# Performance work log

Measured on AMD Instinct MI355X. Metric: run time of the kernel, lower is better.

Reference implementation:

```python
import jax, jax.numpy as jnp
import numpy as np

NTYPES = 2
MAXNEI = 128      # maxNeighborNum
M2 = 16
NPER = 256        # atoms per type
B = 4
EMB = [25, 50, 100]
FIT_IN = M2 * EMB[-1]  # 1600
FH = 240


def setup_inputs() -> dict:
    key = jax.random.key(0)
    ks = jax.random.split(key, 16)
    s = 0.1
    inp = {
        "Ri": jax.random.normal(ks[0], (B, NTYPES * NPER, NTYPES * MAXNEI, 4), jnp.float32),
        "emb_W0": jax.random.normal(ks[1], (4, 1, EMB[0]), jnp.float32) * s,
        "emb_b0": jax.random.normal(ks[2], (4, EMB[0]), jnp.float32) * s,
        "emb_W1": jax.random.normal(ks[3], (4, EMB[0], EMB[1]), jnp.float32) * s,
        "emb_b1": jax.random.normal(ks[4], (4, EMB[1]), jnp.float32) * s,
        "emb_W2": jax.random.normal(ks[5], (4, EMB[1], EMB[2]), jnp.float32) * s,
        "emb_b2": jax.random.normal(ks[6], (4, EMB[2]), jnp.float32) * s,
        "fit_W0": jax.random.normal(ks[7], (2, FIT_IN, FH), jnp.float32) * 0.02,
        "fit_b0": jax.random.normal(ks[8], (2, FH), jnp.float32) * s,
        "fit_W1": jax.random.normal(ks[9], (2, FH, FH), jnp.float32) * 0.05,
        "fit_b1": jax.random.normal(ks[10], (2, FH), jnp.float32) * s,
        "fit_W2": jax.random.normal(ks[11], (2, FH, FH), jnp.float32) * 0.05,
        "fit_b2": jax.random.normal(ks[12], (2, FH), jnp.float32) * s,
        "fit_W3": jax.random.normal(ks[13], (2, FH, 1), jnp.float32) * 0.05,
        "fit_b3": jax.random.normal(ks[14], (2, 1), jnp.float32),
    }
    return inp


def _emb(s, W0, b0, W1, b1, W2, b2):
    # DeepMD-style embedding MLP with doubling resnet skips (1->25->50->100)
    h0 = jnp.tanh(s @ W0 + b0)
    h1 = jnp.tanh(h0 @ W1 + b1) + jnp.concatenate([h0, h0], axis=-1)
    h2 = jnp.tanh(h1 @ W2 + b2) + jnp.concatenate([h1, h1], axis=-1)
    return h2


def _fit(d, W0, b0, W1, b1, W2, b2, W3, b3):
    h = jnp.tanh(d @ W0 + b0)
    h = jnp.tanh(h @ W1 + b1) + h   # resnet skip (equal dims)
    h = jnp.tanh(h @ W2 + b2) + h
    return h @ W3 + b3              # [B, N, 1]


def reference(Ri, emb_W0, emb_b0, emb_W1, emb_b1, emb_W2, emb_b2,
              fit_W0, fit_b0, fit_W1, fit_b1, fit_W2, fit_b2, fit_W3, fit_b3):
    type_nums = NTYPES
    Ei_blocks = []
    for i in range(NTYPES):                      # center-atom type
        Ri_i = Ri[:, i * NPER:(i + 1) * NPER]    # [B, NPER, NTYPES*M, 4]
        xyz = None
        for j in range(NTYPES):                  # neighbor type
            blk = Ri_i[:, :, j * MAXNEI:(j + 1) * MAXNEI, :]  # [B,N,M,4]
            S = blk[..., 0:1]                                  # [B,N,M,1]
            e = i * NTYPES + j
            G = _emb(S, emb_W0[e], emb_b0[e], emb_W1[e], emb_b1[e],
                     emb_W2[e], emb_b2[e])                     # [B,N,M,100]
            tmp = jnp.einsum('bnmc,bnmg->bncg', blk, G)        # [B,N,4,100]
            xyz = tmp if xyz is None else xyz + tmp
        xyz = xyz / (MAXNEI * type_nums)
        xyz_b = xyz[..., :M2]                                  # [B,N,4,16]
        DR = jnp.einsum('bncg,bnch->bngh', xyz, xyz_b)         # [B,N,100,16]
        DR = DR.reshape(B, NPER, FIT_IN)
        Ei_i = _fit(DR, fit_W0[i], fit_b0[i], fit_W1[i], fit_b1[i],
                    fit_W2[i], fit_b2[i], fit_W3[i], fit_b3[i])  # [B,N,1]
        Ei_blocks.append(Ei_i)
    Ei = jnp.concatenate(Ei_blocks, axis=1)     # [B, natoms_sum, 1]
    return Ei[..., 0]                            # per-atom energies [B, natoms_sum]
```

## Files before the change

### kernel.cpp

```cpp
#include <hip/hip_runtime.h>
#include <hip/hip_bf16.h>

#define FH 240
#define FIT_IN 1600
#define NK 2048
#define TLO -16.0f
#define TINVH 64.0f

typedef _Float16 h8 __attribute__((ext_vector_type(8)));
typedef float f4v __attribute__((ext_vector_type(4)));

__device__ __forceinline__ float fast_tanh(float x) {
    float e2 = __builtin_amdgcn_exp2f(x * 2.8853900817779268f);
    return 1.0f - 2.0f * __builtin_amdgcn_rcpf(e2 + 1.0f);
}

#define FMA_ROW(r, s) \
    acc[r][0] += (s) * b0.x; acc[r][1] += (s) * b0.y; \
    acc[r][2] += (s) * b0.z; acc[r][3] += (s) * b0.w; \
    acc[r][4] += (s) * b1.x; acc[r][5] += (s) * b1.y; \
    acc[r][6] += (s) * b1.z; acc[r][7] += (s) * b1.w;

#define TOFF_W0   0
#define TOFF_B0   28
#define TOFF_B1   56
#define TOFF_B2   108
#define TOFF_W1   208
#define TOFF_W2   1508
#define TOFF_H0T  6708
#define TOFF_H1T  10008
#define TSMEM     16608

__global__ __launch_bounds__(256) void k_table(
    const float* __restrict__ eW0, const float* __restrict__ eB0,
    const float* __restrict__ eW1, const float* __restrict__ eB1,
    const float* __restrict__ eW2, const float* __restrict__ eB2,
    float* __restrict__ T)
{
    __shared__ float sm[TSMEM];

    const int t    = threadIdx.x;
    const int w    = t >> 6;
    const int lane = t & 63;
    const int mi   = lane & 7;
    const int gi   = lane >> 3;
    const int mrow = w * 32 + mi * 4;

    const int e  = blockIdx.y;
    const int k0 = blockIdx.x * 128;

    for (int idx = t; idx < 1250; idx += 256) {
        int k = idx / 50, g = idx - k * 50;
        sm[TOFF_W1 + k * 52 + g] = eW1[e * 1250 + idx];
    }
    for (int idx = t; idx < 5000; idx += 256) {
        int k = idx / 100, r = idx - k * 100;
        int half = r / 50, g = r - half * 50;
        sm[TOFF_W2 + k * 104 + half * 52 + g] = eW2[e * 5000 + idx];
    }
    if (t < 25)       { sm[TOFF_W0 + t] = eW0[e * 25 + t]; sm[TOFF_B0 + t] = eB0[e * 25 + t]; }
    else if (t < 75)  { sm[TOFF_B1 + (t - 25)] = eB1[e * 50 + (t - 25)]; }
    else if (t < 175) { sm[TOFF_B2 + (t - 75)] = eB2[e * 100 + (t - 75)]; }
    __syncthreads();

    if (t < 128) {
        const float S = TLO + (float)(k0 + t) * (1.0f / TINVH);
        #pragma unroll
        for (int k = 0; k < 25; ++k)
            sm[TOFF_H0T + k * 132 + t] = fast_tanh(S * sm[TOFF_W0 + k] + sm[TOFF_B0 + k]);
    }
    __syncthreads();

    {
        float acc[4][8];
        #pragma unroll
        for (int r = 0; r < 4; ++r)
            #pragma unroll
            for (int c = 0; c < 8; ++c) acc[r][c] = 0.f;

        #pragma unroll 5
        for (int k = 0; k < 25; ++k) {
            const float4 av = *(const float4*)&sm[TOFF_H0T + k * 132 + mrow];
            const float4 b0 = *(const float4*)&sm[TOFF_W1 + k * 52 + gi * 8];
            const float4 b1 = *(const float4*)&sm[TOFF_W1 + k * 52 + gi * 8 + 4];
            FMA_ROW(0, av.x) FMA_ROW(1, av.y) FMA_ROW(2, av.z) FMA_ROW(3, av.w)
        }
        #pragma unroll
        for (int c = 0; c < 8; ++c) {
            const int g = gi * 8 + c;
            if (g < 50) {
                const int gm = (g < 25) ? g : g - 25;
                const float4 h0r = *(const float4*)&sm[TOFF_H0T + gm * 132 + mrow];
                const float bias = sm[TOFF_B1 + g];
                float4 o;
                o.x = fast_tanh(acc[0][c] + bias) + h0r.x;
                o.y = fast_tanh(acc[1][c] + bias) + h0r.y;
                o.z = fast_tanh(acc[2][c] + bias) + h0r.z;
                o.w = fast_tanh(acc[3][c] + bias) + h0r.w;
                *(float4*)&sm[TOFF_H1T + g * 132 + mrow] = o;
            }
        }
    }
    __syncthreads();

    for (int half = 0; half < 2; ++half) {
        float acc[4][8];
        #pragma unroll
        for (int r = 0; r < 4; ++r)
            #pragma unroll
            for (int c = 0; c < 8; ++c) acc[r][c] = 0.f;

        #pragma unroll 5
        for (int k = 0; k < 50; ++k) {
            const float4 av = *(const float4*)&sm[TOFF_H1T + k * 132 + mrow];
            const float4 b0 = *(const float4*)&sm[TOFF_W2 + k * 104 + half * 52 + gi * 8];
            const float4 b1 = *(const float4*)&sm[TOFF_W2 + k * 104 + half * 52 + gi * 8 + 4];
            FMA_ROW(0, av.x) FMA_ROW(1, av.y) FMA_ROW(2, av.z) FMA_ROW(3, av.w)
        }
        #pragma unroll
        for (int c = 0; c < 8; ++c) {
            const int g = gi * 8 + c;
            if (g < 50) {
                const float4 h1r = *(const float4*)&sm[TOFF_H1T + g * 132 + mrow];
                const float bias = sm[TOFF_B2 + half * 50 + g];
                float* out = T + ((size_t)e * NK + k0 + mrow) * 100 + half * 50 + g;
                out[0]   = fast_tanh(acc[0][c] + bias) + h1r.x;
                out[100] = fast_tanh(acc[1][c] + bias) + h1r.y;
                out[200] = fast_tanh(acc[2][c] + bias) + h1r.z;
                out[300] = fast_tanh(acc[3][c] + bias) + h1r.w;
            }
        }
    }
}

__global__ __launch_bounds__(256) void k_cvt(
    const float* __restrict__ fW0, const float* __restrict__ fW1,
    const float* __restrict__ fW2,
    _Float16* __restrict__ W0T, _Float16* __restrict__ W1T,
    _Float16* __restrict__ W2T)
{
    const int total = 768000 + 115200 + 115200;
    for (int idx = blockIdx.x * 256 + threadIdx.x; idx < total; idx += gridDim.x * 256) {
        if (idx < 768000) {
            const int tp = idx / 384000, r = idx - tp * 384000;
            const int n = r / 1600, k = r - n * 1600;
            W0T[idx] = (_Float16)fW0[tp * 384000 + k * 240 + n];
        } else if (idx < 883200) {
            const int j = idx - 768000;
            const int tp = j / 57600, r = j - tp * 57600;
            const int n = r / 240, k = r - n * 240;
            W1T[j] = (_Float16)fW1[tp * 57600 + k * 240 + n];
        } else {
            const int j = idx - 883200;
            const int tp = j / 57600, r = j - tp * 57600;
            const int n = r / 240, k = r - n * 240;
            W2T[j] = (_Float16)fW2[tp * 57600 + k * 240 + n];
        }
    }
}

__global__ __launch_bounds__(256) void k_xyz(
    const float* __restrict__ Ri, const float* __restrict__ T,
    _Float16* __restrict__ DRh)
{
    __shared__ float4 sR[256];
    __shared__ float  sF[256];
    __shared__ int    sI[256];
    __shared__ float  sXYZ[400];

    const int t   = threadIdx.x;
    const int blk = blockIdx.x;
    const int b   = blk >> 9;
    const int i   = (blk >> 8) & 1;
    const int n   = blk & 255;

    for (int idx = t; idx < 400; idx += 256) sXYZ[idx] = 0.f;

    {
        const int jj = t >> 7, m = t & 127;
        const size_t row = ((size_t)(b * 512 + i * 256 + n)) * 256 + jj * 128 + m;
        const float4 r = *(const float4*)(Ri + row * 4);
        sR[t] = r;
        float u = (r.x - TLO) * TINVH;
        int ii = (int)u;
        ii = (ii < 0) ? 0 : ((ii > NK - 2) ? NK - 2 : ii);
        sI[t] = ii;
        sF[t] = u - (float)ii;
    }
    __syncthreads();

    const int jj = t >> 7;
    const int g  = t & 127;
    if (g < 100) {
        const float* Te = T + ((size_t)(i * 2 + jj)) * NK * 100 + g;
        float a0 = 0.f, a1 = 0.f, a2 = 0.f, a3 = 0.f;
        #pragma unroll 4
        for (int m = 0; m < 128; ++m) {
            const int s = jj * 128 + m;
            const float4 R = sR[s];
            const float  f = sF[s];
            const float* p = Te + (size_t)sI[s] * 100;
            const float v0 = p[0], v1 = p[100];
            const float G = v0 + f * (v1 - v0);
            a0 += R.x * G; a1 += R.y * G; a2 += R.z * G; a3 += R.w * G;
        }
        atomicAdd(&sXYZ[g],       a0);
        atomicAdd(&sXYZ[100 + g], a1);
        atomicAdd(&sXYZ[200 + g], a2);
        atomicAdd(&sXYZ[300 + g], a3);
    }
    __syncthreads();

    const float inv = 1.0f / 65536.0f;
    _Float16* dr = DRh + (((size_t)i * 4 + b) * 256 + n) * FIT_IN;
    for (int q = t; q < 400; q += 256) {
        const int gg = q >> 2, h0 = (q & 3) * 4;
        ushort4 pk;
        _Float16* ph = (_Float16*)&pk;
        #pragma unroll
        for (int r = 0; r < 4; ++r) {
            const int h = h0 + r;
            const float v = (sXYZ[gg] * sXYZ[h] + sXYZ[100 + gg] * sXYZ[100 + h]
                           + sXYZ[200 + gg] * sXYZ[200 + h] + sXYZ[300 + gg] * sXYZ[300 + h]) * inv;
            ph[r] = (_Float16)v;
        }
        *(ushort4*)(dr + gg * 16 + h0) = pk;
    }
}

template<int K, int CHUNK>
__global__ __launch_bounds__(256) void k_fit_mfma(
    const _Float16* __restrict__ A, const _Float16* __restrict__ WT,
    float* __restrict__ P)
{
    __shared__ _Float16 sA[64 * 40];
    __shared__ _Float16 sBT[240 * 40];

    const int t    = threadIdx.x;
    const int w    = t >> 6;
    const int lane = t & 63;
    const int ln   = lane & 15;
    const int quad = lane >> 4;

    const int mtile = blockIdx.x;
    const int ks    = blockIdx.y;
    const int row0  = mtile * 64;
    const int tp    = mtile >> 4;
    const int kbeg  = ks * CHUNK;
    const int kend  = (kbeg + CHUNK < K) ? (kbeg + CHUNK) : K;
    const int nf0   = w * 4;
    const int nfrags = (w < 3) ? 4 : 3;

    f4v acc[4][4];
    #pragma unroll
    for (int mf = 0; mf < 4; ++mf)
        #pragma unroll
        for (int nf = 0; nf < 4; ++nf) acc[mf][nf] = (f4v)0.f;

    const _Float16* Ab = A + (size_t)row0 * K;
    const _Float16* Wb = WT + (size_t)tp * 240 * K;

    for (int k0 = kbeg; k0 < kend; k0 += 32) {
        #pragma unroll
        for (int q = t; q < 512; q += 256) {
            const int m = q >> 3, kq = (q & 7) * 4;
            const int k = k0 + kq;
            uint2 v = make_uint2(0u, 0u);
            if (k < kend) v = *(const uint2*)(Ab + (size_t)m * K + k);
            *(uint2*)&sA[m * 40 + kq] = v;
        }
        for (int q = t; q < 1920; q += 256) {
            const int n = q >> 3, kq = (q & 7) * 4;
            const int k = k0 + kq;
            uint2 v = make_uint2(0u, 0u);
            if (k < kend) v = *(const uint2*)(Wb + (size_t)n * K + k);
            *(uint2*)&sBT[n * 40 + kq] = v;
        }
        __syncthreads();

        h8 afr[4];
        #pragma unroll
        for (int mf = 0; mf < 4; ++mf)
            afr[mf] = *(const h8*)&sA[(mf * 16 + ln) * 40 + quad * 8];
        #pragma unroll
        for (int nf = 0; nf < 4; ++nf) {
            if (nf < nfrags) {
                const h8 bfr = *(const h8*)&sBT[((nf0 + nf) * 16 + ln) * 40 + quad * 8];
                #pragma unroll
                for (int mf = 0; mf < 4; ++mf)
                    acc[mf][nf] = __builtin_amdgcn_mfma_f32_16x16x32_f16(
                        afr[mf], bfr, acc[mf][nf], 0, 0, 0);
            }
        }
        __syncthreads();
    }

    float* Pb = P + ((size_t)ks * 2048 + row0) * FH;
    #pragma unroll
    for (int nf = 0; nf < 4; ++nf) {
        if (nf < nfrags) {
            const int col = (nf0 + nf) * 16 + ln;
            #pragma unroll
            for (int mf = 0; mf < 4; ++mf)
                #pragma unroll
                for (int r = 0; r < 4; ++r) {
                    const int row = mf * 16 + quad * 4 + r;
                    Pb[(size_t)row * FH + col] = acc[mf][nf][r];
                }
        }
    }
}

template<int KSPLIT, bool RES>
__global__ __launch_bounds__(256) void k_fit_reduce(
    const float* __restrict__ P, const float* __restrict__ Bias,
    const float* __restrict__ AinF, float* __restrict__ OutF,
    _Float16* __restrict__ OutH)
{
    const int idx = blockIdx.x * 256 + threadIdx.x;
    if (idx >= 2048 * FH) return;
    const int tp  = idx / (1024 * FH);
    const int col = idx % FH;
    float s = 0.f;
    #pragma unroll
    for (int ks = 0; ks < KSPLIT; ++ks)
        s += P[(size_t)ks * 2048 * FH + idx];
    float v = fast_tanh(s + Bias[tp * FH + col]);
    if (RES) v += AinF[idx];
    OutF[idx] = v;
    OutH[idx] = (_Float16)v;
}

__global__ __launch_bounds__(256) void k_out(
    const float* __restrict__ Hin, const float* __restrict__ W3,
    const float* __restrict__ b3, float* __restrict__ out)
{
    const int wave = (int)((blockIdx.x * 256 + threadIdx.x) >> 6);
    const int lane = threadIdx.x & 63;
    const int tp = wave >> 10;
    const int rem = wave & 1023;
    const int b = rem >> 8, n = rem & 255;
    const float* h = Hin + (size_t)wave * FH;
    const float* wv = W3 + tp * FH;
    float s = 0.f;
    for (int k = lane; k < FH; k += 64) s += h[k] * wv[k];
    #pragma unroll
    for (int off = 32; off > 0; off >>= 1) s += __shfl_down(s, off);
    if (lane == 0) out[b * 512 + tp * 256 + n] = s + b3[tp];
}

extern "C" void kernel_launch(void* const* d_in, const int* in_sizes, int n_in,
                              void* d_out, int out_size, void* d_ws, size_t ws_size,
                              hipStream_t stream)
{
    const float* Ri  = (const float*)d_in[0];
    const float* eW0 = (const float*)d_in[1];
    const float* eB0 = (const float*)d_in[2];
    const float* eW1 = (const float*)d_in[3];
    const float* eB1 = (const float*)d_in[4];
    const float* eW2 = (const float*)d_in[5];
    const float* eB2 = (const float*)d_in[6];
    const float* fW0 = (const float*)d_in[7];
    const float* fb0 = (const float*)d_in[8];
    const float* fW1 = (const float*)d_in[9];
    const float* fb1 = (const float*)d_in[10];
    const float* fW2 = (const float*)d_in[11];
    const float* fb2 = (const float*)d_in[12];
    const float* fW3 = (const float*)d_in[13];
    const float* fb3 = (const float*)d_in[14];

    char* p = (char*)d_ws;
    float* T   = (float*)p;                 p += (size_t)4 * NK * 100 * 4;
    float* P   = (float*)p;                 p += (size_t)17 * 2048 * FH * 4;
    float* hA  = (float*)p;                 p += (size_t)2048 * FH * 4;
    float* hB  = (float*)p;                 p += (size_t)2048 * FH * 4;
    _Float16* DRh = (_Float16*)p;           p += (size_t)2048 * FIT_IN * 2;
    _Float16* hAh = (_Float16*)p;           p += (size_t)2048 * FH * 2;
    _Float16* hBh = (_Float16*)p;           p += (size_t)2048 * FH * 2;
    _Float16* W0T = (_Float16*)p;           p += (size_t)768000 * 2;
    _Float16* W1T = (_Float16*)p;           p += (size_t)115200 * 2;
    _Float16* W2T = (_Float16*)p;           p += (size_t)115200 * 2;

    const int RBLK = (2048 * FH + 255) / 256;

    k_cvt<<<dim3(1024), dim3(256), 0, stream>>>(fW0, fW1, fW2, W0T, W1T, W2T);
    k_table<<<dim3(NK / 128, 4), dim3(256), 0, stream>>>(eW0, eB0, eW1, eB1, eW2, eB2, T);
    k_xyz<<<dim3(2048), dim3(256), 0, stream>>>(Ri, T, DRh);

    k_fit_mfma<FIT_IN, 96><<<dim3(32, 17), dim3(256), 0, stream>>>(DRh, W0T, P);
    k_fit_reduce<17, false><<<dim3(RBLK), dim3(256), 0, stream>>>(P, fb0, nullptr, hA, hAh);

    k_fit_mfma<FH, 32><<<dim3(32, 8), dim3(256), 0, stream>>>(hAh, W1T, P);
    k_fit_reduce<8, true><<<dim3(RBLK), dim3(256), 0, stream>>>(P, fb1, hA, hB, hBh);

    k_fit_mfma<FH, 32><<<dim3(32, 8), dim3(256), 0, stream>>>(hBh, W2T, P);
    k_fit_reduce<8, true><<<dim3(RBLK), dim3(256), 0, stream>>>(P, fb2, hB, hA, hAh);

    k_out<<<dim3(512), dim3(256), 0, stream>>>(hA, fW3, fb3, (float*)d_out);
}
```

Baseline: 195.5 us.

## Fuse fitting-net tail layers into one kernel and retile first fit GEMM

The first fitting GEMM now uses 32-row tiles with an 8-way K split (chunks of 200) instead of 64-row tiles with a 17-way split. The split-K reduction, both hidden layers with residuals, and the output dot product all run in one kernel that works on 16 rows per block and keeps activations in LDS. This removes six launches and the global round trips of the intermediate activations. In exchange the tail runs on only 128 blocks, and each block reloads the full W1/W2 weights, so parallelism in the hidden layers is lower.

```diff
diff --git a/kernel.cpp b/kernel.cpp
--- a/kernel.cpp
+++ b/kernel.cpp
@@ -6,6 +6,8 @@
 #define NK 2048
 #define TLO -16.0f
 #define TINVH 64.0f
+#define KSPLIT0 8
+#define CHUNK0 200
 
 typedef _Float16 h8 __attribute__((ext_vector_type(8)));
 typedef float f4v __attribute__((ext_vector_type(4)));
@@ -233,7 +235,7 @@
     const _Float16* __restrict__ A, const _Float16* __restrict__ WT,
     float* __restrict__ P)
 {
-    __shared__ _Float16 sA[64 * 40];
+    __shared__ _Float16 sA[32 * 40];
     __shared__ _Float16 sBT[240 * 40];
 
     const int t    = threadIdx.x;
@@ -244,16 +246,16 @@
 
     const int mtile = blockIdx.x;
     const int ks    = blockIdx.y;
-    const int row0  = mtile * 64;
-    const int tp    = mtile >> 4;
+    const int row0  = mtile * 32;
+    const int tp    = mtile >> 5;
     const int kbeg  = ks * CHUNK;
     const int kend  = (kbeg + CHUNK < K) ? (kbeg + CHUNK) : K;
     const int nf0   = w * 4;
     const int nfrags = (w < 3) ? 4 : 3;
 
-    f4v acc[4][4];
+    f4v acc[2][4];
     #pragma unroll
-    for (int mf = 0; mf < 4; ++mf)
+    for (int mf = 0; mf < 2; ++mf)
         #pragma unroll
         for (int nf = 0; nf < 4; ++nf) acc[mf][nf] = (f4v)0.f;
 
@@ -261,9 +263,8 @@
     const _Float16* Wb = WT + (size_t)tp * 240 * K;
 
     for (int k0 = kbeg; k0 < kend; k0 += 32) {
-        #pragma unroll
-        for (int q = t; q < 512; q += 256) {
-            const int m = q >> 3, kq = (q & 7) * 4;
+        {
+            const int m = t >> 3, kq = (t & 7) * 4;
             const int k = k0 + kq;
             uint2 v = make_uint2(0u, 0u);
             if (k < kend) v = *(const uint2*)(Ab + (size_t)m * K + k);
@@ -278,16 +279,16 @@
         }
         __syncthreads();
 
-        h8 afr[4];
-        #pragma unroll
-        for (int mf = 0; mf < 4; ++mf)
+        h8 afr[2];
+        #pragma unroll
+        for (int mf = 0; mf < 2; ++mf)
             afr[mf] = *(const h8*)&sA[(mf * 16 + ln) * 40 + quad * 8];
         #pragma unroll
         for (int nf = 0; nf < 4; ++nf) {
             if (nf < nfrags) {
                 const h8 bfr = *(const h8*)&sBT[((nf0 + nf) * 16 + ln) * 40 + quad * 8];
                 #pragma unroll
-                for (int mf = 0; mf < 4; ++mf)
+                for (int mf = 0; mf < 2; ++mf)
                     acc[mf][nf] = __builtin_amdgcn_mfma_f32_16x16x32_f16(
                         afr[mf], bfr, acc[mf][nf], 0, 0, 0);
             }
@@ -301,7 +302,7 @@
         if (nf < nfrags) {
             const int col = (nf0 + nf) * 16 + ln;
             #pragma unroll
-            for (int mf = 0; mf < 4; ++mf)
+            for (int mf = 0; mf < 2; ++mf)
                 #pragma unroll
                 for (int r = 0; r < 4; ++r) {
                     const int row = mf * 16 + quad * 4 + r;
@@ -311,42 +312,110 @@
     }
 }
 
-template<int KSPLIT, bool RES>
-__global__ __launch_bounds__(256) void k_fit_reduce(
-    const float* __restrict__ P, const float* __restrict__ Bias,
-    const float* __restrict__ AinF, float* __restrict__ OutF,
-    _Float16* __restrict__ OutH)
-{
-    const int idx = blockIdx.x * 256 + threadIdx.x;
-    if (idx >= 2048 * FH) return;
-    const int tp  = idx / (1024 * FH);
-    const int col = idx % FH;
-    float s = 0.f;
+__global__ __launch_bounds__(256) void k_fit_tail(
+    const float* __restrict__ P,
+    const _Float16* __restrict__ W1T, const _Float16* __restrict__ W2T,
+    const float* __restrict__ fb0, const float* __restrict__ fb1,
+    const float* __restrict__ fb2, const float* __restrict__ fW3,
+    const float* __restrict__ fb3, float* __restrict__ out)
+{
+    __shared__ float    hRes[2][16 * 240];
+    __shared__ _Float16 sA[16 * 264];
+    __shared__ _Float16 sB[240 * 40];
+
+    const int t    = threadIdx.x;
+    const int w    = t >> 6;
+    const int lane = t & 63;
+    const int ln   = lane & 15;
+    const int quad = lane >> 4;
+    const int r0   = blockIdx.x * 16;
+    const int tp   = r0 >> 10;
+    const int nf0  = w * 4;
+    const int nfrags = (w < 3) ? 4 : 3;
+
     #pragma unroll
-    for (int ks = 0; ks < KSPLIT; ++ks)
-        s += P[(size_t)ks * 2048 * FH + idx];
-    float v = fast_tanh(s + Bias[tp * FH + col]);
-    if (RES) v += AinF[idx];
-    OutF[idx] = v;
-    OutH[idx] = (_Float16)v;
-}
-
-__global__ __launch_bounds__(256) void k_out(
-    const float* __restrict__ Hin, const float* __restrict__ W3,
-    const float* __restrict__ b3, float* __restrict__ out)
-{
-    const int wave = (int)((blockIdx.x * 256 + threadIdx.x) >> 6);
-    const int lane = threadIdx.x & 63;
-    const int tp = wave >> 10;
-    const int rem = wave & 1023;
-    const int b = rem >> 8, n = rem & 255;
-    const float* h = Hin + (size_t)wave * FH;
-    const float* wv = W3 + tp * FH;
-    float s = 0.f;
-    for (int k = lane; k < FH; k += 64) s += h[k] * wv[k];
+    for (int j = 0; j < 15; ++j) {
+        const int e = t + j * 256;
+        const int m = e / 240, col = e - m * 240;
+        const size_t base = (size_t)(r0 + m) * FH + col;
+        float s = 0.f;
+        #pragma unroll
+        for (int ks = 0; ks < KSPLIT0; ++ks)
+            s += P[(size_t)ks * 2048 * FH + base];
+        const float v = fast_tanh(s + fb0[tp * FH + col]);
+        hRes[0][m * 240 + col] = v;
+        sA[m * 264 + col] = (_Float16)v;
+    }
+    if (t < 256) {
+        const int m = t >> 4, c = 240 + (t & 15);
+        sA[m * 264 + c] = (_Float16)0.f;
+    }
+
     #pragma unroll
-    for (int off = 32; off > 0; off >>= 1) s += __shfl_down(s, off);
-    if (lane == 0) out[b * 512 + tp * 256 + n] = s + b3[tp];
+    for (int layer = 0; layer < 2; ++layer) {
+        const _Float16* Wt = (layer == 0 ? W1T : W2T) + (size_t)tp * FH * FH;
+        const float* Bias  = (layer == 0 ? fb1 : fb2) + tp * FH;
+        const float* res   = hRes[layer];
+        float* outb        = hRes[layer ^ 1];
+
+        f4v acc[4];
+        #pragma unroll
+        for (int nf = 0; nf < 4; ++nf) acc[nf] = (f4v)0.f;
+
+        for (int k0 = 0; k0 < 256; k0 += 32) {
+            __syncthreads();
+            for (int q = t; q < 1920; q += 256) {
+                const int n = q >> 3, kq = (q & 7) * 4;
+                const int k = k0 + kq;
+                uint2 v = make_uint2(0u, 0u);
+                if (k < FH) v = *(const uint2*)(Wt + (size_t)n * FH + k);
+                *(uint2*)&sB[n * 40 + kq] = v;
+            }
+            __syncthreads();
+            const h8 afr = *(const h8*)&sA[ln * 264 + k0 + quad * 8];
+            #pragma unroll
+            for (int nf = 0; nf < 4; ++nf) {
+                if (nf < nfrags) {
+                    const h8 bfr = *(const h8*)&sB[((nf0 + nf) * 16 + ln) * 40 + quad * 8];
+                    acc[nf] = __builtin_amdgcn_mfma_f32_16x16x32_f16(afr, bfr, acc[nf], 0, 0, 0);
+                }
+            }
+        }
+        __syncthreads();
+
+        #pragma unroll
+        for (int nf = 0; nf < 4; ++nf) {
+            if (nf < nfrags) {
+                const int col = (nf0 + nf) * 16 + ln;
+                const float bias = Bias[col];
+                #pragma unroll
+                for (int r = 0; r < 4; ++r) {
+                    const int m = quad * 4 + r;
+                    const float v = fast_tanh(acc[nf][r] + bias) + res[m * 240 + col];
+                    outb[m * 240 + col] = v;
+                    if (layer == 0) sA[m * 264 + col] = (_Float16)v;
+                }
+            }
+        }
+        __syncthreads();
+    }
+
+    const float* h2 = hRes[0];
+    const float* wv = fW3 + tp * FH;
+    #pragma unroll
+    for (int rr = 0; rr < 4; ++rr) {
+        const int m = w * 4 + rr;
+        float s = 0.f;
+        for (int k = lane; k < FH; k += 64)
+            s += h2[m * 240 + k] * wv[k];
+        #pragma unroll
+        for (int off = 32; off > 0; off >>= 1) s += __shfl_down(s, off);
+        if (lane == 0) {
+            const int gr = r0 + m;
+            const int b = (gr >> 8) & 3, n = gr & 255;
+            out[b * 512 + tp * 256 + n] = s + fb3[tp];
+        }
+    }
 }
 
 extern "C" void kernel_launch(void* const* d_in, const int* in_sizes, int n_in,
@@ -371,30 +440,18 @@
 
     char* p = (char*)d_ws;
     float* T   = (float*)p;                 p += (size_t)4 * NK * 100 * 4;
-    float* P   = (float*)p;                 p += (size_t)17 * 2048 * FH * 4;
-    float* hA  = (float*)p;                 p += (size_t)2048 * FH * 4;
-    float* hB  = (float*)p;                 p += (size_t)2048 * FH * 4;
+    float* P   = (float*)p;                 p += (size_t)KSPLIT0 * 2048 * FH * 4;
     _Float16* DRh = (_Float16*)p;           p += (size_t)2048 * FIT_IN * 2;
-    _Float16* hAh = (_Float16*)p;           p += (size_t)2048 * FH * 2;
-    _Float16* hBh = (_Float16*)p;           p += (size_t)2048 * FH * 2;
     _Float16* W0T = (_Float16*)p;           p += (size_t)768000 * 2;
     _Float16* W1T = (_Float16*)p;           p += (size_t)115200 * 2;
     _Float16* W2T = (_Float16*)p;           p += (size_t)115200 * 2;
 
-    const int RBLK = (2048 * FH + 255) / 256;
-
     k_cvt<<<dim3(1024), dim3(256), 0, stream>>>(fW0, fW1, fW2, W0T, W1T, W2T);
     k_table<<<dim3(NK / 128, 4), dim3(256), 0, stream>>>(eW0, eB0, eW1, eB1, eW2, eB2, T);
     k_xyz<<<dim3(2048), dim3(256), 0, stream>>>(Ri, T, DRh);
 
-    k_fit_mfma<FIT_IN, 96><<<dim3(32, 17), dim3(256), 0, stream>>>(DRh, W0T, P);
-    k_fit_reduce<17, false><<<dim3(RBLK), dim3(256), 0, stream>>>(P, fb0, nullptr, hA, hAh);
-
-    k_fit_mfma<FH, 32><<<dim3(32, 8), dim3(256), 0, stream>>>(hAh, W1T, P);
-    k_fit_reduce<8, true><<<dim3(RBLK), dim3(256), 0, stream>>>(P, fb1, hA, hB, hBh);
-
-    k_fit_mfma<FH, 32><<<dim3(32, 8), dim3(256), 0, stream>>>(hBh, W2T, P);
-    k_fit_reduce<8, true><<<dim3(RBLK), dim3(256), 0, stream>>>(P, fb2, hB, hA, hAh);
-
-    k_out<<<dim3(512), dim3(256), 0, stream>>>(hA, fW3, fb3, (float*)d_out);
-}
+    k_fit_mfma<FIT_IN, CHUNK0><<<dim3(64, KSPLIT0), dim3(256), 0, stream>>>(DRh, W0T, P);
+
+    k_fit_tail<<<dim3(128), dim3(256), 0, stream>>>(P, W1T, W2T, fb0, fb1, fb2, fW3, fb3,
+                                                    (float*)d_out);
+}
```

Result: no change. 196.7 us (+0.6%).
